# Kernel optimization log

Measured on AMD Instinct MI355X. Metric: run time of the kernel, lower is better.

The kernel has to match this reference:

```python
import jax, jax.numpy as jnp
import numpy as np

N, E = 40000, 640000          # nodes, edges (avg degree 16)
IN_N, IN_E = 8 + 768, 2       # in_dim_node + in_dim_text, in_dim_edge
H, OUT, NC, L = 128, 128, 5, 2
EPS_BN, EPS_DEN = 1e-5, 1e-6


def setup_inputs() -> dict:
    key = jax.random.key(0)
    ks = jax.random.split(key, 16)
    w = lambda k, shape: jax.random.normal(k, shape, jnp.float32) * 0.05
    return {
        "node_feat": jax.random.normal(ks[0], (N, IN_N), jnp.float32),
        "edge_feat": jax.random.normal(ks[1], (E, IN_E), jnp.float32),
        "src": jax.random.randint(ks[2], (E,), 0, N),
        "dst": jax.random.randint(ks[3], (E,), 0, N),
        "enc_nw": w(ks[4], (IN_N, H)), "enc_nb": jnp.zeros((H,), jnp.float32),
        "enc_ew": w(ks[5], (IN_E, H)), "enc_eb": jnp.zeros((H,), jnp.float32),
        # per layer: 5 linears (order A, B, C, D, E)
        "lin_w": w(ks[6], (L, 5, H, H)), "lin_b": jnp.zeros((L, 5, H), jnp.float32),
        "bnh_g": jnp.ones((L, H), jnp.float32), "bnh_b": jnp.zeros((L, H), jnp.float32),
        "bne_g": jnp.ones((L, H), jnp.float32), "bne_b": jnp.zeros((L, H), jnp.float32),
        "mlp_w1": w(ks[7], (H, OUT)), "mlp_b1": jnp.zeros((OUT,), jnp.float32),
        "mlp_w2": w(ks[8], (OUT, NC)), "mlp_b2": jnp.zeros((NC,), jnp.float32),
    }


def _bn(x, g, b):
    # training-mode BatchNorm1d: batch stats, biased variance, eps=1e-5
    m = jnp.mean(x, axis=0)
    v = jnp.var(x, axis=0)
    return (x - m) * jax.lax.rsqrt(v + EPS_BN) * g + b


def reference(node_feat, edge_feat, src, dst, enc_nw, enc_nb, enc_ew, enc_eb,
              lin_w, lin_b, bnh_g, bnh_b, bne_g, bne_b,
              mlp_w1, mlp_b1, mlp_w2, mlp_b2):
    n = node_feat.shape[0]
    h = node_feat @ enc_nw + enc_nb          # [N, H]
    e = edge_feat @ enc_ew + enc_eb          # [E, H]
    for l in range(L):
        Ah = h @ lin_w[l, 0] + lin_b[l, 0]
        Bh = h @ lin_w[l, 1] + lin_b[l, 1]
        Ce = e @ lin_w[l, 2] + lin_b[l, 2]
        Dh = h @ lin_w[l, 3] + lin_b[l, 3]
        Eh = h @ lin_w[l, 4] + lin_b[l, 4]
        e_new = Ce + Dh[src] + Eh[dst]       # [E, H] edge gate logits
        sigma = jax.nn.sigmoid(e_new)
        num = jax.ops.segment_sum(sigma * Bh[src], dst, num_segments=n)
        den = jax.ops.segment_sum(sigma, dst, num_segments=n)
        h_new = Ah + num / (den + EPS_DEN)
        h = jax.nn.relu(_bn(h_new, bnh_g[l], bnh_b[l]))
        e = jax.nn.relu(_bn(e_new, bne_g[l], bne_b[l]))
    # MLP readout per node (dropout p=0 -> identity)
    logits = jax.nn.relu(h @ mlp_w1 + mlp_b1) @ mlp_w2 + mlp_b2
    return logits
```

## Files before the change

### kernel.cpp

```cpp
#include <hip/hip_runtime.h>
#include <math.h>

#define NN 40000
#define NE 640000
#define KIN 776
#define HH 128
#define NCLS 5

typedef __attribute__((ext_vector_type(8))) short bf16x8;
typedef __attribute__((ext_vector_type(4))) short bf16x4;
typedef __attribute__((ext_vector_type(4))) float f32x4;

__device__ __forceinline__ float bf2f(short u) {
    return __uint_as_float(((unsigned)(unsigned short)u) << 16);
}
__device__ __forceinline__ short f2bf(float f) {
    unsigned u = __float_as_uint(f);
    u += 0x7fffu + ((u >> 16) & 1u);
    return (short)(u >> 16);
}

enum { A_F32 = 0 };

template<int NSTEP, bool TAIL8>
__global__ __launch_bounds__(256)
void mfma_gemm(const float* __restrict__ Af, const short* __restrict__ Wp,
               const float* __restrict__ bias, short* __restrict__ Cb, int K)
{
    const int lane = threadIdx.x & 63;
    const int wave = threadIdx.x >> 6;
    const int q = lane >> 4;
    const int c16 = lane & 15;
    const int row = blockIdx.x * 64 + wave * 16 + c16;

    f32x4 acc[8];
#pragma unroll
    for (int n = 0; n < 8; ++n) acc[n] = (f32x4){0.f, 0.f, 0.f, 0.f};

    for (int kt = 0; kt < NSTEP; ++kt) {
        bf16x8 afrag;
        const int kbase = kt * 32 + q * 8;
        if (!TAIL8 || kt < NSTEP - 1 || q == 0) {
            const float* p = Af + (size_t)row * K + kbase;
            const float4 x = *(const float4*)p;
            const float4 y = *(const float4*)(p + 4);
            afrag[0] = f2bf(x.x); afrag[1] = f2bf(x.y);
            afrag[2] = f2bf(x.z); afrag[3] = f2bf(x.w);
            afrag[4] = f2bf(y.x); afrag[5] = f2bf(y.y);
            afrag[6] = f2bf(y.z); afrag[7] = f2bf(y.w);
        } else {
#pragma unroll
            for (int j = 0; j < 8; ++j) afrag[j] = 0;
        }
        const int kb = kt * 4 + q;
#pragma unroll
        for (int n = 0; n < 8; ++n) {
            const bf16x8 wfrag =
                *(const bf16x8*)(Wp + (size_t)kb * 1024 + (n * 16 + c16) * 8);
            acc[n] = __builtin_amdgcn_mfma_f32_16x16x32_bf16(wfrag, afrag, acc[n], 0, 0, 0);
        }
    }
#pragma unroll
    for (int n = 0; n < 8; ++n) {
        const int col = n * 16 + q * 4;
        const float4 b4 = *(const float4*)(bias + col);
        bf16x4 o;
        o[0] = f2bf(acc[n][0] + b4.x); o[1] = f2bf(acc[n][1] + b4.y);
        o[2] = f2bf(acc[n][2] + b4.z); o[3] = f2bf(acc[n][3] + b4.w);
        *(bf16x4*)(Cb + (size_t)row * HH + col) = o;
    }
}

__global__ __launch_bounds__(256)
void edge2_k(short* __restrict__ enew, const short* __restrict__ Wp,
             const float* __restrict__ bias, const float* __restrict__ bnp,
             const short* __restrict__ Dh, const short* __restrict__ Eh,
             const int* __restrict__ src_s, const int* __restrict__ dst_s)
{
    const int lane = threadIdx.x & 63;
    const int wave = threadIdx.x >> 6;
    const int q = lane >> 4;
    const int c16 = lane & 15;
    const int row0 = blockIdx.x * 128 + wave * 16 + c16;
    const int row1 = row0 + 64;

    const int s0 = src_s[row0], d0 = dst_s[row0];
    const int s1 = src_s[row1], d1 = dst_s[row1];

    f32x4 acc[2][8];
#pragma unroll
    for (int n = 0; n < 8; ++n) {
        const int col = n * 16 + q * 4;
        const float4 b4 = *(const float4*)(bias + col);
        const bf16x4 dh0 = *(const bf16x4*)(Dh + (size_t)s0 * HH + col);
        const bf16x4 eh0 = *(const bf16x4*)(Eh + (size_t)d0 * HH + col);
        const bf16x4 dh1 = *(const bf16x4*)(Dh + (size_t)s1 * HH + col);
        const bf16x4 eh1 = *(const bf16x4*)(Eh + (size_t)d1 * HH + col);
        const float bb[4] = {b4.x, b4.y, b4.z, b4.w};
#pragma unroll
        for (int j = 0; j < 4; ++j) {
            acc[0][n][j] = bb[j] + bf2f(dh0[j]) + bf2f(eh0[j]);
            acc[1][n][j] = bb[j] + bf2f(dh1[j]) + bf2f(eh1[j]);
        }
    }

#pragma unroll
    for (int kt = 0; kt < 4; ++kt) {
        const int kbase = kt * 32 + q * 8;
        const float4 sc0 = *(const float4*)(bnp + kbase);
        const float4 sc1 = *(const float4*)(bnp + kbase + 4);
        const float4 sh0 = *(const float4*)(bnp + HH + kbase);
        const float4 sh1 = *(const float4*)(bnp + HH + kbase + 4);
        const float scv[8] = {sc0.x, sc0.y, sc0.z, sc0.w, sc1.x, sc1.y, sc1.z, sc1.w};
        const float shv[8] = {sh0.x, sh0.y, sh0.z, sh0.w, sh1.x, sh1.y, sh1.z, sh1.w};
        const bf16x8 r0 = *(const bf16x8*)(enew + (size_t)row0 * HH + kbase);
        const bf16x8 r1 = *(const bf16x8*)(enew + (size_t)row1 * HH + kbase);
        bf16x8 a0, a1;
#pragma unroll
        for (int j = 0; j < 8; ++j) {
            a0[j] = f2bf(fmaxf(fmaf(bf2f(r0[j]), scv[j], shv[j]), 0.f));
            a1[j] = f2bf(fmaxf(fmaf(bf2f(r1[j]), scv[j], shv[j]), 0.f));
        }
        const int kb = kt * 4 + q;
#pragma unroll
        for (int n = 0; n < 8; ++n) {
            const bf16x8 wfrag =
                *(const bf16x8*)(Wp + (size_t)kb * 1024 + (n * 16 + c16) * 8);
            acc[0][n] = __builtin_amdgcn_mfma_f32_16x16x32_bf16(wfrag, a0, acc[0][n], 0, 0, 0);
            acc[1][n] = __builtin_amdgcn_mfma_f32_16x16x32_bf16(wfrag, a1, acc[1][n], 0, 0, 0);
        }
    }

#pragma unroll
    for (int n = 0; n < 8; ++n) {
        const int col = n * 16 + q * 4;
        bf16x4 o0, o1;
#pragma unroll
        for (int j = 0; j < 4; ++j) {
            o0[j] = f2bf(acc[0][n][j]);
            o1[j] = f2bf(acc[1][n][j]);
        }
        *(bf16x4*)(enew + (size_t)row0 * HH + col) = o0;
        *(bf16x4*)(enew + (size_t)row1 * HH + col) = o1;
    }
}

template<bool ABN>
__global__ __launch_bounds__(256, 2)
void fused4_k(const short* __restrict__ hb, const float* __restrict__ hf,
              const float* __restrict__ bnp,
              const short* __restrict__ w0, const short* __restrict__ w1,
              const short* __restrict__ w2, const short* __restrict__ w3,
              const float* __restrict__ b0, const float* __restrict__ b1,
              const float* __restrict__ b2, const float* __restrict__ b3,
              float* __restrict__ Ah, short* __restrict__ Bh,
              short* __restrict__ Dh, short* __restrict__ Eh)
{
    const int lane = threadIdx.x & 63;
    const int wave = threadIdx.x >> 6;
    const int q = lane >> 4;
    const int c16 = lane & 15;
    const int row = blockIdx.x * 64 + wave * 16 + c16;

    f32x4 acc[4][8];
#pragma unroll
    for (int t = 0; t < 4; ++t)
#pragma unroll
        for (int n = 0; n < 8; ++n) acc[t][n] = (f32x4){0.f, 0.f, 0.f, 0.f};

    const short* const ws[4] = {w0, w1, w2, w3};
#pragma unroll
    for (int kt = 0; kt < 4; ++kt) {
        const int kbase = kt * 32 + q * 8;
        bf16x8 afrag;
        if (!ABN) {
            afrag = *(const bf16x8*)(hb + (size_t)row * HH + kbase);
        } else {
            const float* p = hf + (size_t)row * HH + kbase;
            const float4 x = *(const float4*)p;
            const float4 y = *(const float4*)(p + 4);
            const float4 s0 = *(const float4*)(bnp + kbase);
            const float4 s1 = *(const float4*)(bnp + kbase + 4);
            const float4 t0 = *(const float4*)(bnp + HH + kbase);
            const float4 t1 = *(const float4*)(bnp + HH + kbase + 4);
            const float xv[8] = {x.x, x.y, x.z, x.w, y.x, y.y, y.z, y.w};
            const float scv[8] = {s0.x, s0.y, s0.z, s0.w, s1.x, s1.y, s1.z, s1.w};
            const float shv[8] = {t0.x, t0.y, t0.z, t0.w, t1.x, t1.y, t1.z, t1.w};
#pragma unroll
            for (int j = 0; j < 8; ++j)
                afrag[j] = f2bf(fmaxf(fmaf(xv[j], scv[j], shv[j]), 0.f));
        }
        const int kb = kt * 4 + q;
#pragma unroll
        for (int t = 0; t < 4; ++t)
#pragma unroll
            for (int n = 0; n < 8; ++n) {
                const bf16x8 wfrag =
                    *(const bf16x8*)(ws[t] + (size_t)kb * 1024 + (n * 16 + c16) * 8);
                acc[t][n] = __builtin_amdgcn_mfma_f32_16x16x32_bf16(wfrag, afrag, acc[t][n], 0, 0, 0);
            }
    }

    const float* const bs[4] = {b0, b1, b2, b3};
#pragma unroll
    for (int t = 0; t < 4; ++t) {
#pragma unroll
        for (int n = 0; n < 8; ++n) {
            const int col = n * 16 + q * 4;
            const float4 b4 = *(const float4*)(bs[t] + col);
            const float v[4] = {acc[t][n][0] + b4.x, acc[t][n][1] + b4.y,
                                acc[t][n][2] + b4.z, acc[t][n][3] + b4.w};
            if (t == 0) {
                *(float4*)(Ah + (size_t)row * HH + col) = make_float4(v[0], v[1], v[2], v[3]);
            } else {
                bf16x4 o;
#pragma unroll
                for (int j = 0; j < 4; ++j) o[j] = f2bf(v[j]);
                short* dstp = (t == 1) ? Bh : ((t == 2) ? Dh : Eh);
                *(bf16x4*)(dstp + (size_t)row * HH + col) = o;
            }
        }
    }
}

__global__ __launch_bounds__(256)
void readout_k(const float* __restrict__ hnew, const float* __restrict__ bnp,
               const short* __restrict__ Wp, const float* __restrict__ b1,
               const float* __restrict__ w2, const float* __restrict__ b2,
               float* __restrict__ out)
{
    const int lane = threadIdx.x & 63;
    const int wave = threadIdx.x >> 6;
    const int q = lane >> 4;
    const int c16 = lane & 15;
    const int row = blockIdx.x * 64 + wave * 16 + c16;

    f32x4 acc[8];
#pragma unroll
    for (int n = 0; n < 8; ++n) acc[n] = (f32x4){0.f, 0.f, 0.f, 0.f};

#pragma unroll
    for (int kt = 0; kt < 4; ++kt) {
        const int kbase = kt * 32 + q * 8;
        const float* p = hnew + (size_t)row * HH + kbase;
        const float4 x = *(const float4*)p;
        const float4 y = *(const float4*)(p + 4);
        const float4 s0 = *(const float4*)(bnp + kbase);
        const float4 s1 = *(const float4*)(bnp + kbase + 4);
        const float4 t0 = *(const float4*)(bnp + HH + kbase);
        const float4 t1 = *(const float4*)(bnp + HH + kbase + 4);
        const float xv[8] = {x.x, x.y, x.z, x.w, y.x, y.y, y.z, y.w};
        const float scv[8] = {s0.x, s0.y, s0.z, s0.w, s1.x, s1.y, s1.z, s1.w};
        const float shv[8] = {t0.x, t0.y, t0.z, t0.w, t1.x, t1.y, t1.z, t1.w};
        bf16x8 afrag;
#pragma unroll
        for (int j = 0; j < 8; ++j)
            afrag[j] = f2bf(fmaxf(fmaf(xv[j], scv[j], shv[j]), 0.f));
        const int kb = kt * 4 + q;
#pragma unroll
        for (int n = 0; n < 8; ++n) {
            const bf16x8 wfrag =
                *(const bf16x8*)(Wp + (size_t)kb * 1024 + (n * 16 + c16) * 8);
            acc[n] = __builtin_amdgcn_mfma_f32_16x16x32_bf16(wfrag, afrag, acc[n], 0, 0, 0);
        }
    }

    float part[NCLS] = {};
#pragma unroll
    for (int n = 0; n < 8; ++n) {
        const int col = n * 16 + q * 4;
        const float4 b4 = *(const float4*)(b1 + col);
        const float bb[4] = {b4.x, b4.y, b4.z, b4.w};
#pragma unroll
        for (int j = 0; j < 4; ++j) {
            const float zv = fmaxf(acc[n][j] + bb[j], 0.f);
#pragma unroll
            for (int t = 0; t < NCLS; ++t)
                part[t] = fmaf(zv, w2[(col + j) * NCLS + t], part[t]);
        }
    }
#pragma unroll
    for (int t = 0; t < NCLS; ++t) {
        part[t] += __shfl_xor(part[t], 16, 64);
        part[t] += __shfl_xor(part[t], 32, 64);
    }
    if (q == 0) {
#pragma unroll
        for (int t = 0; t < NCLS; ++t)
            out[(size_t)row * NCLS + t] = part[t] + b2[t];
    }
}

__global__ __launch_bounds__(256)
void prepack_k(const float* __restrict__ enc_nw, const float* __restrict__ lin_w,
               const float* __restrict__ mlp_w1, short* __restrict__ wp)
{
    const int t = blockIdx.x * 256 + threadIdx.x;
    if (t >= 260 * 128) return;
    const int kbg = t >> 7, col = t & 127;
    const int kb0[11]  = {0, 100, 116, 132, 148, 164, 180, 196, 212, 228, 244};
    const int psel[11] = {0, 1, 1, 1, 1, 1, 1, 1, 1, 1, 2};
    const int soff[11] = {0, 0 * 16384, 1 * 16384, 3 * 16384, 4 * 16384,
                          5 * 16384, 6 * 16384, 7 * 16384, 8 * 16384, 9 * 16384, 0};
    const int Ksrc[11] = {KIN, 128, 128, 128, 128, 128, 128, 128, 128, 128, 128};
    int e = 10;
    while (e > 0 && kbg < kb0[e]) --e;
    const float* base = (psel[e] == 0) ? enc_nw : ((psel[e] == 1) ? lin_w : mlp_w1);
    const int kbl = kbg - kb0[e];
    bf16x8 o;
#pragma unroll
    for (int j = 0; j < 8; ++j) {
        const int k = kbl * 8 + j;
        const float v = (k < Ksrc[e]) ? base[(size_t)soff[e] + (size_t)k * HH + col] : 0.f;
        o[j] = f2bf(v);
    }
    *(bf16x8*)(wp + (size_t)kbg * 1024 + col * 8) = o;
}

__global__ void gpre_k(const float* __restrict__ enc_ew, const float* __restrict__ enc_eb,
                       const float* __restrict__ Wc, const float* __restrict__ bc,
                       float* __restrict__ G)
{
    const int c = threadIdx.x;
    float a0 = 0.f, a1 = 0.f, ab = 0.f;
    for (int k = 0; k < HH; ++k) {
        const float w = Wc[k * HH + c];
        a0 = fmaf(enc_ew[k], w, a0);
        a1 = fmaf(enc_ew[HH + k], w, a1);
        ab = fmaf(enc_eb[k], w, ab);
    }
    G[c] = a0; G[HH + c] = a1; G[2 * HH + c] = ab + bc[c];
}

__global__ __launch_bounds__(256)
void edge1_k(const float* __restrict__ ef, const int* __restrict__ eidx,
             const int* __restrict__ src_s, const int* __restrict__ dst_s,
             const float* __restrict__ G,
             const short* __restrict__ Dh, const short* __restrict__ Eh,
             short* __restrict__ enew, float* __restrict__ pbuf)
{
    const int tid = threadIdx.x;
    const int er = tid >> 4, cg = tid & 15;
    const int col = cg * 8;
    const float4 g00 = *(const float4*)(G + col);
    const float4 g01 = *(const float4*)(G + col + 4);
    const float4 g10 = *(const float4*)(G + HH + col);
    const float4 g11 = *(const float4*)(G + HH + col + 4);
    const float4 gb0 = *(const float4*)(G + 2 * HH + col);
    const float4 gb1 = *(const float4*)(G + 2 * HH + col + 4);
    const float G0v[8] = {g00.x, g00.y, g00.z, g00.w, g01.x, g01.y, g01.z, g01.w};
    const float G1v[8] = {g10.x, g10.y, g10.z, g10.w, g11.x, g11.y, g11.z, g11.w};
    const float GBv[8] = {gb0.x, gb0.y, gb0.z, gb0.w, gb1.x, gb1.y, gb1.z, gb1.w};
    float sa[8] = {}, qa[8] = {};
    for (int it = 0; it < 16; ++it) {
        const int i = blockIdx.x * 256 + it * 16 + er;
        const int e = eidx[i];
        const float f0 = ef[(size_t)e * 2];
        const float f1 = ef[(size_t)e * 2 + 1];
        const int s = src_s[i], d = dst_s[i];
        const bf16x8 dh = *(const bf16x8*)(Dh + (size_t)s * HH + col);
        const bf16x8 eh = *(const bf16x8*)(Eh + (size_t)d * HH + col);
        bf16x8 o;
#pragma unroll
        for (int j = 0; j < 8; ++j) {
            const float v = fmaf(f0, G0v[j], fmaf(f1, G1v[j], GBv[j]))
                            + bf2f(dh[j]) + bf2f(eh[j]);
            sa[j] += v; qa[j] += v * v;
            o[j] = f2bf(v);
        }
        *(bf16x8*)(enew + (size_t)i * HH + col) = o;
    }
    __shared__ float sred[16][136];
    const int slot = (blockIdx.x & 63) * 256;
#pragma unroll
    for (int j = 0; j < 8; ++j) sred[er][col + j] = sa[j];
    __syncthreads();
    for (int s2 = 8; s2 > 0; s2 >>= 1) {
        if (er < s2)
#pragma unroll
            for (int j = 0; j < 8; ++j) sred[er][col + j] += sred[er + s2][col + j];
        __syncthreads();
    }
    if (er == 0)
#pragma unroll
        for (int j = 0; j < 8; ++j) atomicAdd(pbuf + slot + col + j, sred[0][col + j]);
    __syncthreads();
#pragma unroll
    for (int j = 0; j < 8; ++j) sred[er][col + j] = qa[j];
    __syncthreads();
    for (int s2 = 8; s2 > 0; s2 >>= 1) {
        if (er < s2)
#pragma unroll
            for (int j = 0; j < 8; ++j) sred[er][col + j] += sred[er + s2][col + j];
        __syncthreads();
    }
    if (er == 0)
#pragma unroll
        for (int j = 0; j < 8; ++j) atomicAdd(pbuf + slot + 128 + col + j, sred[0][col + j]);
}

__global__ __launch_bounds__(256)
void hist_k(const int* __restrict__ dst, int* __restrict__ cnt)
{
    const int e = blockIdx.x * 256 + threadIdx.x;
    if (e < NE) atomicAdd(cnt + dst[e], 1);
}

__global__ __launch_bounds__(1024)
void scan_k(const int* __restrict__ cnt, int* __restrict__ rowptr, int* __restrict__ wr)
{
    __shared__ int s[1024];
    const int t = threadIdx.x;
    const int base = t * 40;
    int sum = 0;
    for (int i = 0; i < 40; ++i) {
        const int idx = base + i;
        if (idx < NN) sum += cnt[idx];
    }
    s[t] = sum;
    __syncthreads();
    for (int off = 1; off < 1024; off <<= 1) {
        const int v = (t >= off) ? s[t - off] : 0;
        __syncthreads();
        s[t] += v;
        __syncthreads();
    }
    int run = (t == 0) ? 0 : s[t - 1];
    for (int i = 0; i < 40; ++i) {
        const int idx = base + i;
        if (idx < NN) {
            rowptr[idx] = run;
            wr[idx] = run;
            run += cnt[idx];
        }
    }
    if (t == 1023) rowptr[NN] = s[1023];
}

__global__ __launch_bounds__(256)
void scatter_k2(const int* __restrict__ dst, const int* __restrict__ src,
                int* __restrict__ wr, int* __restrict__ eidx,
                int* __restrict__ src_s, int* __restrict__ dst_s)
{
    const int e = blockIdx.x * 256 + threadIdx.x;
    if (e < NE) {
        const int d = dst[e];
        const int p = atomicAdd(wr + d, 1);
        eidx[p] = e;
        src_s[p] = src[e];
        dst_s[p] = d;
    }
}

__global__ __launch_bounds__(256)
void seg_reduce_v(const short* __restrict__ enew, const int* __restrict__ rowptr,
                  const int* __restrict__ src_s, const short* __restrict__ Bh,
                  const float* __restrict__ Ah, float* __restrict__ hnew,
                  float* __restrict__ pbuf)
{
    const int wv = threadIdx.x >> 6;
    const int lane = threadIdx.x & 63;
    const int slot = lane >> 4;
    const int cg = lane & 15;
    const int col = cg * 8;
    const int n0 = (blockIdx.x * 4 + wv) * 8;
    float sa[8] = {}, qa[8] = {};
    for (int nn = 0; nn < 8; ++nn) {
        const int n = n0 + nn;
        const int k0 = rowptr[n], k1 = rowptr[n + 1];
        float num[8] = {}, den[8] = {};
        for (int k = k0 + slot; k < k1; k += 4) {
            const bf16x8 ev = *(const bf16x8*)(enew + (size_t)k * HH + col);
            const int s = src_s[k];
            const bf16x8 bv = *(const bf16x8*)(Bh + (size_t)s * HH + col);
#pragma unroll
            for (int j = 0; j < 8; ++j) {
                const float sg = 1.f / (1.f + __expf(-bf2f(ev[j])));
                den[j] += sg;
                num[j] = fmaf(sg, bf2f(bv[j]), num[j]);
            }
        }
#pragma unroll
        for (int j = 0; j < 8; ++j) {
            num[j] += __shfl_xor(num[j], 16, 64);
            den[j] += __shfl_xor(den[j], 16, 64);
            num[j] += __shfl_xor(num[j], 32, 64);
            den[j] += __shfl_xor(den[j], 32, 64);
        }
        if (slot == 0) {
            const size_t idx = (size_t)n * HH + col;
            const float4 a0 = *(const float4*)(Ah + idx);
            const float4 a1 = *(const float4*)(Ah + idx + 4);
            const float av[8] = {a0.x, a0.y, a0.z, a0.w, a1.x, a1.y, a1.z, a1.w};
            float x[8];
#pragma unroll
            for (int j = 0; j < 8; ++j) {
                x[j] = av[j] + num[j] / (den[j] + 1e-6f);
                sa[j] += x[j]; qa[j] += x[j] * x[j];
            }
            *(float4*)(hnew + idx) = make_float4(x[0], x[1], x[2], x[3]);
            *(float4*)(hnew + idx + 4) = make_float4(x[4], x[5], x[6], x[7]);
        }
    }
    if (slot == 0) {
        const int sl = (blockIdx.x & 63) * 256;
#pragma unroll
        for (int j = 0; j < 8; ++j) {
            atomicAdd(pbuf + sl + col + j, sa[j]);
            atomicAdd(pbuf + sl + 128 + col + j, qa[j]);
        }
    }
}

__global__ void make_bnp2(const float* __restrict__ pbuf, const float* __restrict__ g,
                          const float* __restrict__ b, float cntInv,
                          float* __restrict__ out)
{
    const int c = threadIdx.x;
    float s = 0.f, q = 0.f;
    for (int i = 0; i < 64; ++i) {
        s += pbuf[i * 256 + c];
        q += pbuf[i * 256 + 128 + c];
    }
    const float m = s * cntInv;
    const float var = q * cntInv - m * m;
    const float rs = rsqrtf(var + 1e-5f);
    const float sc = g[c] * rs;
    out[c] = sc;
    out[128 + c] = b[c] - m * sc;
}

extern "C" void kernel_launch(void* const* d_in, const int* in_sizes, int n_in,
                              void* d_out, int out_size, void* d_ws, size_t ws_size,
                              hipStream_t stream)
{
    const float* node_feat = (const float*)d_in[0];
    const float* edge_feat = (const float*)d_in[1];
    const int*   src       = (const int*)d_in[2];
    const int*   dst       = (const int*)d_in[3];
    const float* enc_nw    = (const float*)d_in[4];
    const float* enc_nb    = (const float*)d_in[5];
    const float* enc_ew    = (const float*)d_in[6];
    const float* enc_eb    = (const float*)d_in[7];
    const float* lin_w     = (const float*)d_in[8];
    const float* lin_b     = (const float*)d_in[9];
    const float* bnh_g     = (const float*)d_in[10];
    const float* bnh_b     = (const float*)d_in[11];
    const float* bne_g     = (const float*)d_in[12];
    const float* bne_b     = (const float*)d_in[13];
    const float* mlp_w1    = (const float*)d_in[14];
    const float* mlp_b1    = (const float*)d_in[15];
    const float* mlp_w2    = (const float*)d_in[16];
    const float* mlp_b2    = (const float*)d_in[17];
    float* out = (float*)d_out;

    char* base = (char*)d_ws;
    size_t off = 0;
    auto alloc = [&](size_t bytes) -> void* {
        void* p = base + off;
        off = (off + bytes + 255) & ~(size_t)255;
        return p;
    };
    const size_t NH = (size_t)NN * HH;
    float* hnew  = (float*)alloc(NH * 4);
    float* Ah    = (float*)alloc(NH * 4);
    short* h0    = (short*)alloc(NH * 2);
    short* Bh    = (short*)alloc(NH * 2);
    short* Dh    = (short*)alloc(NH * 2);
    short* Eh    = (short*)alloc(NH * 2);
    short* enew  = (short*)alloc((size_t)NE * HH * 2);
    short* wpack = (short*)alloc((size_t)260 * 1024 * 2);
    float* G     = (float*)alloc(384 * 4);
    float* bnpe  = (float*)alloc(256 * 4);
    float* bnph  = (float*)alloc(256 * 4);
    float* pbe   = (float*)alloc(16384 * 4);
    float* pbh0  = (float*)alloc(16384 * 4);
    float* pbh1  = (float*)alloc(16384 * 4);
    int* cnt     = (int*)alloc(NN * 4);
    int* rowptr  = (int*)alloc((NN + 1) * 4);
    int* wr      = (int*)alloc(NN * 4);
    int* eidx    = (int*)alloc((size_t)NE * 4);
    int* src_s   = (int*)alloc((size_t)NE * 4);
    int* dst_s   = (int*)alloc((size_t)NE * 4);

    const dim3 blk(256);

    hipMemsetAsync(cnt, 0, NN * 4, stream);
    hipMemsetAsync(pbe, 0, 3 * 16384 * 4, stream);
    hist_k<<<2500, blk, 0, stream>>>(dst, cnt);
    scan_k<<<1, 1024, 0, stream>>>(cnt, rowptr, wr);
    scatter_k2<<<2500, blk, 0, stream>>>(dst, src, wr, eidx, src_s, dst_s);
    prepack_k<<<130, blk, 0, stream>>>(enc_nw, lin_w, mlp_w1, wpack);
    gpre_k<<<1, 128, 0, stream>>>(enc_ew, enc_eb, lin_w + 2 * 16384, lin_b + 2 * HH, G);

    mfma_gemm<25, true><<<625, blk, 0, stream>>>(node_feat, wpack, enc_nb, h0, KIN);

    {
        const float* Bv = lin_b;
        fused4_k<false><<<625, blk, 0, stream>>>(
            h0, nullptr, nullptr,
            wpack + (size_t)100 * 1024, wpack + (size_t)116 * 1024,
            wpack + (size_t)132 * 1024, wpack + (size_t)148 * 1024,
            Bv + 0 * HH, Bv + 1 * HH, Bv + 3 * HH, Bv + 4 * HH,
            Ah, Bh, Dh, Eh);
        edge1_k<<<2500, blk, 0, stream>>>(edge_feat, eidx, src_s, dst_s, G,
                                          Dh, Eh, enew, pbe);
        make_bnp2<<<1, 128, 0, stream>>>(pbe, bne_g, bne_b, 1.f / NE, bnpe);
        seg_reduce_v<<<1250, blk, 0, stream>>>(enew, rowptr, src_s, Bh, Ah, hnew, pbh0);
        make_bnp2<<<1, 128, 0, stream>>>(pbh0, bnh_g, bnh_b, 1.f / NN, bnph);
    }

    {
        const float* Bv = lin_b + 5 * HH;
        fused4_k<true><<<625, blk, 0, stream>>>(
            nullptr, hnew, bnph,
            wpack + (size_t)164 * 1024, wpack + (size_t)180 * 1024,
            wpack + (size_t)212 * 1024, wpack + (size_t)228 * 1024,
            Bv + 0 * HH, Bv + 1 * HH, Bv + 3 * HH, Bv + 4 * HH,
            Ah, Bh, Dh, Eh);
        edge2_k<<<5000, blk, 0, stream>>>(enew, wpack + (size_t)196 * 1024,
                                          Bv + 2 * HH, bnpe, Dh, Eh, src_s, dst_s);
        seg_reduce_v<<<1250, blk, 0, stream>>>(enew, rowptr, src_s, Bh, Ah, hnew, pbh1);
        make_bnp2<<<1, 128, 0, stream>>>(pbh1, bnh_g + HH, bnh_b + HH, 1.f / NN, bnph);
    }

    readout_k<<<625, blk, 0, stream>>>(hnew, bnph, wpack + (size_t)244 * 1024,
                                       mlp_b1, mlp_w2, mlp_b2, out);
}
```

Baseline: 816.0 us.

## Fuse edge gate computation with destination segment reduction per node

The edge-logit kernels are merged with the segmented sum/sigmoid aggregation. Each wave walks a node's incoming edges in CSR order, builds e_new and accumulates num/den right away. This avoids a second full read of the E×H edge tensor in layer 1 and avoids writing it at all in layer 2. It also removes the dst_s array, and the node BN statistics move to a separate small hstats kernel. In exchange, layer 2's MFMA now runs on 16-edge chunks per node, so low-degree nodes waste lanes on padding, and load balance follows the degree distribution.

```diff
diff --git a/kernel.cpp b/kernel.cpp
--- a/kernel.cpp
+++ b/kernel.cpp
@@ -19,8 +19,6 @@
     u += 0x7fffu + ((u >> 16) & 1u);
     return (short)(u >> 16);
 }
-
-enum { A_F32 = 0 };
 
 template<int NSTEP, bool TAIL8>
 __global__ __launch_bounds__(256)
@@ -68,80 +66,6 @@
         o[0] = f2bf(acc[n][0] + b4.x); o[1] = f2bf(acc[n][1] + b4.y);
         o[2] = f2bf(acc[n][2] + b4.z); o[3] = f2bf(acc[n][3] + b4.w);
         *(bf16x4*)(Cb + (size_t)row * HH + col) = o;
-    }
-}
-
-__global__ __launch_bounds__(256)
-void edge2_k(short* __restrict__ enew, const short* __restrict__ Wp,
-             const float* __restrict__ bias, const float* __restrict__ bnp,
-             const short* __restrict__ Dh, const short* __restrict__ Eh,
-             const int* __restrict__ src_s, const int* __restrict__ dst_s)
-{
-    const int lane = threadIdx.x & 63;
-    const int wave = threadIdx.x >> 6;
-    const int q = lane >> 4;
-    const int c16 = lane & 15;
-    const int row0 = blockIdx.x * 128 + wave * 16 + c16;
-    const int row1 = row0 + 64;
-
-    const int s0 = src_s[row0], d0 = dst_s[row0];
-    const int s1 = src_s[row1], d1 = dst_s[row1];
-
-    f32x4 acc[2][8];
-#pragma unroll
-    for (int n = 0; n < 8; ++n) {
-        const int col = n * 16 + q * 4;
-        const float4 b4 = *(const float4*)(bias + col);
-        const bf16x4 dh0 = *(const bf16x4*)(Dh + (size_t)s0 * HH + col);
-        const bf16x4 eh0 = *(const bf16x4*)(Eh + (size_t)d0 * HH + col);
-        const bf16x4 dh1 = *(const bf16x4*)(Dh + (size_t)s1 * HH + col);
-        const bf16x4 eh1 = *(const bf16x4*)(Eh + (size_t)d1 * HH + col);
-        const float bb[4] = {b4.x, b4.y, b4.z, b4.w};
-#pragma unroll
-        for (int j = 0; j < 4; ++j) {
-            acc[0][n][j] = bb[j] + bf2f(dh0[j]) + bf2f(eh0[j]);
-            acc[1][n][j] = bb[j] + bf2f(dh1[j]) + bf2f(eh1[j]);
-        }
-    }
-
-#pragma unroll
-    for (int kt = 0; kt < 4; ++kt) {
-        const int kbase = kt * 32 + q * 8;
-        const float4 sc0 = *(const float4*)(bnp + kbase);
-        const float4 sc1 = *(const float4*)(bnp + kbase + 4);
-        const float4 sh0 = *(const float4*)(bnp + HH + kbase);
-        const float4 sh1 = *(const float4*)(bnp + HH + kbase + 4);
-        const float scv[8] = {sc0.x, sc0.y, sc0.z, sc0.w, sc1.x, sc1.y, sc1.z, sc1.w};
-        const float shv[8] = {sh0.x, sh0.y, sh0.z, sh0.w, sh1.x, sh1.y, sh1.z, sh1.w};
-        const bf16x8 r0 = *(const bf16x8*)(enew + (size_t)row0 * HH + kbase);
-        const bf16x8 r1 = *(const bf16x8*)(enew + (size_t)row1 * HH + kbase);
-        bf16x8 a0, a1;
-#pragma unroll
-        for (int j = 0; j < 8; ++j) {
-            a0[j] = f2bf(fmaxf(fmaf(bf2f(r0[j]), scv[j], shv[j]), 0.f));
-            a1[j] = f2bf(fmaxf(fmaf(bf2f(r1[j]), scv[j], shv[j]), 0.f));
-        }
-        const int kb = kt * 4 + q;
-#pragma unroll
-        for (int n = 0; n < 8; ++n) {
-            const bf16x8 wfrag =
-                *(const bf16x8*)(Wp + (size_t)kb * 1024 + (n * 16 + c16) * 8);
-            acc[0][n] = __builtin_amdgcn_mfma_f32_16x16x32_bf16(wfrag, a0, acc[0][n], 0, 0, 0);
-            acc[1][n] = __builtin_amdgcn_mfma_f32_16x16x32_bf16(wfrag, a1, acc[1][n], 0, 0, 0);
-        }
-    }
-
-#pragma unroll
-    for (int n = 0; n < 8; ++n) {
-        const int col = n * 16 + q * 4;
-        bf16x4 o0, o1;
-#pragma unroll
-        for (int j = 0; j < 4; ++j) {
-            o0[j] = f2bf(acc[0][n][j]);
-            o1[j] = f2bf(acc[1][n][j]);
-        }
-        *(bf16x4*)(enew + (size_t)row0 * HH + col) = o0;
-        *(bf16x4*)(enew + (size_t)row1 * HH + col) = o1;
     }
 }
 
@@ -224,6 +148,216 @@
 }
 
 __global__ __launch_bounds__(256)
+void edge1seg_k(const float* __restrict__ ef, const int* __restrict__ eidx,
+                const int* __restrict__ src_s, const int* __restrict__ rowptr,
+                const float* __restrict__ G,
+                const short* __restrict__ Dh, const short* __restrict__ Eh,
+                const short* __restrict__ Bh, const float* __restrict__ Ah,
+                short* __restrict__ enew, float* __restrict__ hnew,
+                float* __restrict__ pbuf)
+{
+    const int wv = threadIdx.x >> 6;
+    const int lane = threadIdx.x & 63;
+    const int slot = lane >> 4;
+    const int cg = lane & 15;
+    const int col = cg * 8;
+    const int n0 = (blockIdx.x * 4 + wv) * 8;
+
+    const float4 g00 = *(const float4*)(G + col);
+    const float4 g01 = *(const float4*)(G + col + 4);
+    const float4 g10 = *(const float4*)(G + HH + col);
+    const float4 g11 = *(const float4*)(G + HH + col + 4);
+    const float4 gb0 = *(const float4*)(G + 2 * HH + col);
+    const float4 gb1 = *(const float4*)(G + 2 * HH + col + 4);
+    const float G0v[8] = {g00.x, g00.y, g00.z, g00.w, g01.x, g01.y, g01.z, g01.w};
+    const float G1v[8] = {g10.x, g10.y, g10.z, g10.w, g11.x, g11.y, g11.z, g11.w};
+    const float GBv[8] = {gb0.x, gb0.y, gb0.z, gb0.w, gb1.x, gb1.y, gb1.z, gb1.w};
+
+    float esa[8] = {}, esq[8] = {};
+
+    for (int nn = 0; nn < 8; ++nn) {
+        const int n = n0 + nn;
+        const int k0 = rowptr[n], k1 = rowptr[n + 1];
+        const bf16x8 ehn = *(const bf16x8*)(Eh + (size_t)n * HH + col);
+        float ehv[8];
+#pragma unroll
+        for (int j = 0; j < 8; ++j) ehv[j] = bf2f(ehn[j]);
+        float num[8] = {}, den[8] = {};
+        for (int k = k0 + slot; k < k1; k += 4) {
+            const int e = eidx[k];
+            const int s = src_s[k];
+            const float f0 = ef[(size_t)e * 2];
+            const float f1 = ef[(size_t)e * 2 + 1];
+            const bf16x8 dh = *(const bf16x8*)(Dh + (size_t)s * HH + col);
+            const bf16x8 bh = *(const bf16x8*)(Bh + (size_t)s * HH + col);
+            bf16x8 o;
+#pragma unroll
+            for (int j = 0; j < 8; ++j) {
+                const float v = fmaf(f0, G0v[j], fmaf(f1, G1v[j], GBv[j]))
+                                + bf2f(dh[j]) + ehv[j];
+                o[j] = f2bf(v);
+                esa[j] += v; esq[j] += v * v;
+                const float sg = 1.f / (1.f + __expf(-v));
+                den[j] += sg;
+                num[j] = fmaf(sg, bf2f(bh[j]), num[j]);
+            }
+            *(bf16x8*)(enew + (size_t)k * HH + col) = o;
+        }
+#pragma unroll
+        for (int j = 0; j < 8; ++j) {
+            num[j] += __shfl_xor(num[j], 16, 64);
+            den[j] += __shfl_xor(den[j], 16, 64);
+            num[j] += __shfl_xor(num[j], 32, 64);
+            den[j] += __shfl_xor(den[j], 32, 64);
+        }
+        if (slot == 0) {
+            const size_t idx = (size_t)n * HH + col;
+            const float4 a0 = *(const float4*)(Ah + idx);
+            const float4 a1 = *(const float4*)(Ah + idx + 4);
+            const float av[8] = {a0.x, a0.y, a0.z, a0.w, a1.x, a1.y, a1.z, a1.w};
+            float x[8];
+#pragma unroll
+            for (int j = 0; j < 8; ++j) x[j] = av[j] + num[j] / (den[j] + 1e-6f);
+            *(float4*)(hnew + idx) = make_float4(x[0], x[1], x[2], x[3]);
+            *(float4*)(hnew + idx + 4) = make_float4(x[4], x[5], x[6], x[7]);
+        }
+    }
+
+    __shared__ float sred[16][136];
+    const int er = threadIdx.x >> 4;
+    const int slotp = (blockIdx.x & 63) * 256;
+#pragma unroll
+    for (int j = 0; j < 8; ++j) sred[er][col + j] = esa[j];
+    __syncthreads();
+    for (int s2 = 8; s2 > 0; s2 >>= 1) {
+        if (er < s2)
+#pragma unroll
+            for (int j = 0; j < 8; ++j) sred[er][col + j] += sred[er + s2][col + j];
+        __syncthreads();
+    }
+    if (er == 0)
+#pragma unroll
+        for (int j = 0; j < 8; ++j) atomicAdd(pbuf + slotp + col + j, sred[0][col + j]);
+    __syncthreads();
+#pragma unroll
+    for (int j = 0; j < 8; ++j) sred[er][col + j] = esq[j];
+    __syncthreads();
+    for (int s2 = 8; s2 > 0; s2 >>= 1) {
+        if (er < s2)
+#pragma unroll
+            for (int j = 0; j < 8; ++j) sred[er][col + j] += sred[er + s2][col + j];
+        __syncthreads();
+    }
+    if (er == 0)
+#pragma unroll
+        for (int j = 0; j < 8; ++j) atomicAdd(pbuf + slotp + 128 + col + j, sred[0][col + j]);
+}
+
+__global__ __launch_bounds__(256)
+void edge2seg_k(const short* __restrict__ enew, const short* __restrict__ Wp,
+                const float* __restrict__ bias, const float* __restrict__ bnp,
+                const short* __restrict__ Dh, const short* __restrict__ Eh,
+                const short* __restrict__ Bh, const int* __restrict__ src_s,
+                const int* __restrict__ rowptr, const float* __restrict__ Ah,
+                float* __restrict__ hnew)
+{
+    const int wv = threadIdx.x >> 6;
+    const int lane = threadIdx.x & 63;
+    const int q = lane >> 4;
+    const int c16 = lane & 15;
+    const int n0 = (blockIdx.x * 4 + wv) * 8;
+
+    for (int nn = 0; nn < 8; ++nn) {
+        const int n = n0 + nn;
+        const int k0 = rowptr[n], k1 = rowptr[n + 1];
+        float num[8][4] = {}, den[8][4] = {};
+        const int nch = (k1 - k0 + 15) >> 4;
+        for (int ch = 0; ch < nch; ++ch) {
+            const int k = k0 + ch * 16 + c16;
+            const bool valid = (k < k1);
+            const int kr = valid ? k : k0;
+            const int s = src_s[kr];
+
+            f32x4 acc[8];
+#pragma unroll
+            for (int n8 = 0; n8 < 8; ++n8) {
+                const int col = n8 * 16 + q * 4;
+                const float4 b4 = *(const float4*)(bias + col);
+                const bf16x4 dh = *(const bf16x4*)(Dh + (size_t)s * HH + col);
+                const bf16x4 eh = *(const bf16x4*)(Eh + (size_t)n * HH + col);
+                const float bb[4] = {b4.x, b4.y, b4.z, b4.w};
+#pragma unroll
+                for (int j = 0; j < 4; ++j)
+                    acc[n8][j] = bb[j] + bf2f(dh[j]) + bf2f(eh[j]);
+            }
+
+#pragma unroll
+            for (int kt = 0; kt < 4; ++kt) {
+                const int kbase = kt * 32 + q * 8;
+                const float4 sc0 = *(const float4*)(bnp + kbase);
+                const float4 sc1 = *(const float4*)(bnp + kbase + 4);
+                const float4 sh0 = *(const float4*)(bnp + HH + kbase);
+                const float4 sh1 = *(const float4*)(bnp + HH + kbase + 4);
+                const float scv[8] = {sc0.x, sc0.y, sc0.z, sc0.w, sc1.x, sc1.y, sc1.z, sc1.w};
+                const float shv[8] = {sh0.x, sh0.y, sh0.z, sh0.w, sh1.x, sh1.y, sh1.z, sh1.w};
+                const bf16x8 raw = *(const bf16x8*)(enew + (size_t)kr * HH + kbase);
+                bf16x8 afrag;
+#pragma unroll
+                for (int j = 0; j < 8; ++j)
+                    afrag[j] = f2bf(fmaxf(fmaf(bf2f(raw[j]), scv[j], shv[j]), 0.f));
+                const int kb = kt * 4 + q;
+#pragma unroll
+                for (int n8 = 0; n8 < 8; ++n8) {
+                    const bf16x8 wfrag =
+                        *(const bf16x8*)(Wp + (size_t)kb * 1024 + (n8 * 16 + c16) * 8);
+                    acc[n8] = __builtin_amdgcn_mfma_f32_16x16x32_bf16(wfrag, afrag, acc[n8], 0, 0, 0);
+                }
+            }
+
+#pragma unroll
+            for (int n8 = 0; n8 < 8; ++n8) {
+                const int col = n8 * 16 + q * 4;
+                const bf16x4 bh = *(const bf16x4*)(Bh + (size_t)s * HH + col);
+                if (valid) {
+#pragma unroll
+                    for (int j = 0; j < 4; ++j) {
+                        const float sg = 1.f / (1.f + __expf(-acc[n8][j]));
+                        den[n8][j] += sg;
+                        num[n8][j] = fmaf(sg, bf2f(bh[j]), num[n8][j]);
+                    }
+                }
+            }
+        }
+
+#pragma unroll
+        for (int n8 = 0; n8 < 8; ++n8)
+#pragma unroll
+            for (int j = 0; j < 4; ++j) {
+                float nv = num[n8][j], dv = den[n8][j];
+                nv += __shfl_xor(nv, 1, 64);  dv += __shfl_xor(dv, 1, 64);
+                nv += __shfl_xor(nv, 2, 64);  dv += __shfl_xor(dv, 2, 64);
+                nv += __shfl_xor(nv, 4, 64);  dv += __shfl_xor(dv, 4, 64);
+                nv += __shfl_xor(nv, 8, 64);  dv += __shfl_xor(dv, 8, 64);
+                num[n8][j] = nv; den[n8][j] = dv;
+            }
+        if (c16 == 0) {
+#pragma unroll
+            for (int n8 = 0; n8 < 8; ++n8) {
+                const int col = n8 * 16 + q * 4;
+                const size_t idx = (size_t)n * HH + col;
+                const float4 a4 = *(const float4*)(Ah + idx);
+                const float av[4] = {a4.x, a4.y, a4.z, a4.w};
+                float x[4];
+#pragma unroll
+                for (int j = 0; j < 4; ++j)
+                    x[j] = av[j] + num[n8][j] / (den[n8][j] + 1e-6f);
+                *(float4*)(hnew + idx) = make_float4(x[0], x[1], x[2], x[3]);
+            }
+        }
+    }
+}
+
+__global__ __launch_bounds__(256)
 void readout_k(const float* __restrict__ hnew, const float* __restrict__ bnp,
                const short* __restrict__ Wp, const float* __restrict__ b1,
                const float* __restrict__ w2, const float* __restrict__ b2,
@@ -333,73 +467,6 @@
 }
 
 __global__ __launch_bounds__(256)
-void edge1_k(const float* __restrict__ ef, const int* __restrict__ eidx,
-             const int* __restrict__ src_s, const int* __restrict__ dst_s,
-             const float* __restrict__ G,
-             const short* __restrict__ Dh, const short* __restrict__ Eh,
-             short* __restrict__ enew, float* __restrict__ pbuf)
-{
-    const int tid = threadIdx.x;
-    const int er = tid >> 4, cg = tid & 15;
-    const int col = cg * 8;
-    const float4 g00 = *(const float4*)(G + col);
-    const float4 g01 = *(const float4*)(G + col + 4);
-    const float4 g10 = *(const float4*)(G + HH + col);
-    const float4 g11 = *(const float4*)(G + HH + col + 4);
-    const float4 gb0 = *(const float4*)(G + 2 * HH + col);
-    const float4 gb1 = *(const float4*)(G + 2 * HH + col + 4);
-    const float G0v[8] = {g00.x, g00.y, g00.z, g00.w, g01.x, g01.y, g01.z, g01.w};
-    const float G1v[8] = {g10.x, g10.y, g10.z, g10.w, g11.x, g11.y, g11.z, g11.w};
-    const float GBv[8] = {gb0.x, gb0.y, gb0.z, gb0.w, gb1.x, gb1.y, gb1.z, gb1.w};
-    float sa[8] = {}, qa[8] = {};
-    for (int it = 0; it < 16; ++it) {
-        const int i = blockIdx.x * 256 + it * 16 + er;
-        const int e = eidx[i];
-        const float f0 = ef[(size_t)e * 2];
-        const float f1 = ef[(size_t)e * 2 + 1];
-        const int s = src_s[i], d = dst_s[i];
-        const bf16x8 dh = *(const bf16x8*)(Dh + (size_t)s * HH + col);
-        const bf16x8 eh = *(const bf16x8*)(Eh + (size_t)d * HH + col);
-        bf16x8 o;
-#pragma unroll
-        for (int j = 0; j < 8; ++j) {
-            const float v = fmaf(f0, G0v[j], fmaf(f1, G1v[j], GBv[j]))
-                            + bf2f(dh[j]) + bf2f(eh[j]);
-            sa[j] += v; qa[j] += v * v;
-            o[j] = f2bf(v);
-        }
-        *(bf16x8*)(enew + (size_t)i * HH + col) = o;
-    }
-    __shared__ float sred[16][136];
-    const int slot = (blockIdx.x & 63) * 256;
-#pragma unroll
-    for (int j = 0; j < 8; ++j) sred[er][col + j] = sa[j];
-    __syncthreads();
-    for (int s2 = 8; s2 > 0; s2 >>= 1) {
-        if (er < s2)
-#pragma unroll
-            for (int j = 0; j < 8; ++j) sred[er][col + j] += sred[er + s2][col + j];
-        __syncthreads();
-    }
-    if (er == 0)
-#pragma unroll
-        for (int j = 0; j < 8; ++j) atomicAdd(pbuf + slot + col + j, sred[0][col + j]);
-    __syncthreads();
-#pragma unroll
-    for (int j = 0; j < 8; ++j) sred[er][col + j] = qa[j];
-    __syncthreads();
-    for (int s2 = 8; s2 > 0; s2 >>= 1) {
-        if (er < s2)
-#pragma unroll
-            for (int j = 0; j < 8; ++j) sred[er][col + j] += sred[er + s2][col + j];
-        __syncthreads();
-    }
-    if (er == 0)
-#pragma unroll
-        for (int j = 0; j < 8; ++j) atomicAdd(pbuf + slot + 128 + col + j, sred[0][col + j]);
-}
-
-__global__ __launch_bounds__(256)
 void hist_k(const int* __restrict__ dst, int* __restrict__ cnt)
 {
     const int e = blockIdx.x * 256 + threadIdx.x;
@@ -438,9 +505,9 @@
 }
 
 __global__ __launch_bounds__(256)
-void scatter_k2(const int* __restrict__ dst, const int* __restrict__ src,
-                int* __restrict__ wr, int* __restrict__ eidx,
-                int* __restrict__ src_s, int* __restrict__ dst_s)
+void scatter_k(const int* __restrict__ dst, const int* __restrict__ src,
+               int* __restrict__ wr, int* __restrict__ eidx,
+               int* __restrict__ src_s)
 {
     const int e = blockIdx.x * 256 + threadIdx.x;
     if (e < NE) {
@@ -448,68 +515,28 @@
         const int p = atomicAdd(wr + d, 1);
         eidx[p] = e;
         src_s[p] = src[e];
-        dst_s[p] = d;
-    }
-}
-
-__global__ __launch_bounds__(256)
-void seg_reduce_v(const short* __restrict__ enew, const int* __restrict__ rowptr,
-                  const int* __restrict__ src_s, const short* __restrict__ Bh,
-                  const float* __restrict__ Ah, float* __restrict__ hnew,
-                  float* __restrict__ pbuf)
-{
-    const int wv = threadIdx.x >> 6;
-    const int lane = threadIdx.x & 63;
-    const int slot = lane >> 4;
-    const int cg = lane & 15;
-    const int col = cg * 8;
-    const int n0 = (blockIdx.x * 4 + wv) * 8;
-    float sa[8] = {}, qa[8] = {};
-    for (int nn = 0; nn < 8; ++nn) {
-        const int n = n0 + nn;
-        const int k0 = rowptr[n], k1 = rowptr[n + 1];
-        float num[8] = {}, den[8] = {};
-        for (int k = k0 + slot; k < k1; k += 4) {
-            const bf16x8 ev = *(const bf16x8*)(enew + (size_t)k * HH + col);
-            const int s = src_s[k];
-            const bf16x8 bv = *(const bf16x8*)(Bh + (size_t)s * HH + col);
-#pragma unroll
-            for (int j = 0; j < 8; ++j) {
-                const float sg = 1.f / (1.f + __expf(-bf2f(ev[j])));
-                den[j] += sg;
-                num[j] = fmaf(sg, bf2f(bv[j]), num[j]);
-            }
-        }
-#pragma unroll
-        for (int j = 0; j < 8; ++j) {
-            num[j] += __shfl_xor(num[j], 16, 64);
-            den[j] += __shfl_xor(den[j], 16, 64);
-            num[j] += __shfl_xor(num[j], 32, 64);
-            den[j] += __shfl_xor(den[j], 32, 64);
-        }
-        if (slot == 0) {
-            const size_t idx = (size_t)n * HH + col;
-            const float4 a0 = *(const float4*)(Ah + idx);
-            const float4 a1 = *(const float4*)(Ah + idx + 4);
-            const float av[8] = {a0.x, a0.y, a0.z, a0.w, a1.x, a1.y, a1.z, a1.w};
-            float x[8];
-#pragma unroll
-            for (int j = 0; j < 8; ++j) {
-                x[j] = av[j] + num[j] / (den[j] + 1e-6f);
-                sa[j] += x[j]; qa[j] += x[j] * x[j];
-            }
-            *(float4*)(hnew + idx) = make_float4(x[0], x[1], x[2], x[3]);
-            *(float4*)(hnew + idx + 4) = make_float4(x[4], x[5], x[6], x[7]);
-        }
-    }
-    if (slot == 0) {
-        const int sl = (blockIdx.x & 63) * 256;
-#pragma unroll
-        for (int j = 0; j < 8; ++j) {
-            atomicAdd(pbuf + sl + col + j, sa[j]);
-            atomicAdd(pbuf + sl + 128 + col + j, qa[j]);
-        }
-    }
+    }
+}
+
+__global__ __launch_bounds__(256)
+void hstats_k(const float* __restrict__ hnew, float* __restrict__ pbuf)
+{
+    const int tid = threadIdx.x;
+    const int c = tid & 127, sub = tid >> 7;
+    const int r0 = blockIdx.x * 256;
+    float sa = 0.f, qa = 0.f;
+    for (int i = sub; i < 256; i += 2) {
+        const int r = r0 + i;
+        if (r >= NN) break;
+        const float x = hnew[(size_t)r * HH + c];
+        sa += x; qa += x * x;
+    }
+    __shared__ float red[256];
+    red[tid] = sa; __syncthreads();
+    if (tid < 128) atomicAdd(pbuf + (blockIdx.x & 63) * 256 + c, red[tid] + red[tid + 128]);
+    __syncthreads();
+    red[tid] = qa; __syncthreads();
+    if (tid < 128) atomicAdd(pbuf + (blockIdx.x & 63) * 256 + 128 + c, red[tid] + red[tid + 128]);
 }
 
 __global__ void make_bnp2(const float* __restrict__ pbuf, const float* __restrict__ g,
@@ -581,7 +608,6 @@
     int* wr      = (int*)alloc(NN * 4);
     int* eidx    = (int*)alloc((size_t)NE * 4);
     int* src_s   = (int*)alloc((size_t)NE * 4);
-    int* dst_s   = (int*)alloc((size_t)NE * 4);
 
     const dim3 blk(256);
 
@@ -589,7 +615,7 @@
     hipMemsetAsync(pbe, 0, 3 * 16384 * 4, stream);
     hist_k<<<2500, blk, 0, stream>>>(dst, cnt);
     scan_k<<<1, 1024, 0, stream>>>(cnt, rowptr, wr);
-    scatter_k2<<<2500, blk, 0, stream>>>(dst, src, wr, eidx, src_s, dst_s);
+    scatter_k<<<2500, blk, 0, stream>>>(dst, src, wr, eidx, src_s);
     prepack_k<<<130, blk, 0, stream>>>(enc_nw, lin_w, mlp_w1, wpack);
     gpre_k<<<1, 128, 0, stream>>>(enc_ew, enc_eb, lin_w + 2 * 16384, lin_b + 2 * HH, G);
 
@@ -603,10 +629,10 @@
             wpack + (size_t)132 * 1024, wpack + (size_t)148 * 1024,
             Bv + 0 * HH, Bv + 1 * HH, Bv + 3 * HH, Bv + 4 * HH,
             Ah, Bh, Dh, Eh);
-        edge1_k<<<2500, blk, 0, stream>>>(edge_feat, eidx, src_s, dst_s, G,
-                                          Dh, Eh, enew, pbe);
+        edge1seg_k<<<1250, blk, 0, stream>>>(edge_feat, eidx, src_s, rowptr, G,
+                                             Dh, Eh, Bh, Ah, enew, hnew, pbe);
         make_bnp2<<<1, 128, 0, stream>>>(pbe, bne_g, bne_b, 1.f / NE, bnpe);
-        seg_reduce_v<<<1250, blk, 0, stream>>>(enew, rowptr, src_s, Bh, Ah, hnew, pbh0);
+        hstats_k<<<157, blk, 0, stream>>>(hnew, pbh0);
         make_bnp2<<<1, 128, 0, stream>>>(pbh0, bnh_g, bnh_b, 1.f / NN, bnph);
     }
 
@@ -618,9 +644,10 @@
             wpack + (size_t)212 * 1024, wpack + (size_t)228 * 1024,
             Bv + 0 * HH, Bv + 1 * HH, Bv + 3 * HH, Bv + 4 * HH,
             Ah, Bh, Dh, Eh);
-        edge2_k<<<5000, blk, 0, stream>>>(enew, wpack + (size_t)196 * 1024,
-                                          Bv + 2 * HH, bnpe, Dh, Eh, src_s, dst_s);
-        seg_reduce_v<<<1250, blk, 0, stream>>>(enew, rowptr, src_s, Bh, Ah, hnew, pbh1);
+        edge2seg_k<<<1250, blk, 0, stream>>>(enew, wpack + (size_t)196 * 1024,
+                                             Bv + 2 * HH, bnpe, Dh, Eh, Bh,
+                                             src_s, rowptr, Ah, hnew);
+        hstats_k<<<157, blk, 0, stream>>>(hnew, pbh1);
         make_bnp2<<<1, 128, 0, stream>>>(pbh1, bnh_g + HH, bnh_b + HH, 1.f / NN, bnph);
     }
 
```

Measured after the change: 1.200 ms. 47.0% more time.
